# Performance work log

Measured on AMD Instinct MI355X. Metric: run time of the kernel, lower is better.

Reference implementation:

```python
import jax, jax.numpy as jnp
import numpy as np

B, T, L, D = 4, 64, 4096, 4096
MASK_VALUE = -1000000000.0


def setup_inputs() -> dict:
    key = jax.random.key(0)
    kq, km, ka = jax.random.split(key, 3)
    Q = jax.random.normal(kq, (1, T, D), dtype=jnp.float32)          # learned queries
    mask = jax.random.normal(km, (B, L, D), dtype=jnp.float32)       # acts as K and V
    attn_mask = jax.random.randint(ka, (B, T, L), 0, 2).astype(bool)  # True -> masked
    return {"mask": mask, "Q": Q, "attn_mask": attn_mask}


def reference(mask, Q, attn_mask):
    # scores: [B, T, L] = Q @ mask^T / sqrt(D)   (Q broadcast over batch)
    scale = 1.0 / np.sqrt(D).astype(np.float32)
    scores = jnp.einsum('td,bld->btl', Q[0], mask) * scale
    scores = jnp.where(attn_mask, MASK_VALUE, scores)
    attn = jax.nn.softmax(scores, axis=-1)
    # context: [B, T, D] = attn @ mask
    context = jnp.einsum('btl,bld->btd', attn, mask)
    return context
```

## Files before the change

### kernel.cpp

```cpp
#include <hip/hip_runtime.h>
#include <hip/hip_bf16.h>
#include <stdint.h>

#define B_ 4
#define T_ 64
#define L_ 4096
#define D_ 4096

using bf8   = __attribute__((ext_vector_type(8))) short;
using f32x4 = __attribute__((ext_vector_type(4))) float;

__device__ __forceinline__ unsigned short f2bf(float f) {
    union { float f; unsigned int u; } v;
    v.f = f;
    unsigned int r = v.u + 0x7fffu + ((v.u >> 16) & 1u);
    return (unsigned short)(r >> 16);
}

__device__ __forceinline__ int swz16(int row, int byteoff) {
    return byteoff ^ (((row ^ (row >> 3)) & 7) << 4);
}

__device__ __forceinline__ bf8 read_frag(const unsigned short* lds, int row, int kk, int lane) {
    int byte = kk * 64 + ((lane >> 4) << 4);
    int off  = row * 128 + swz16(row, byte);
    return *reinterpret_cast<const bf8*>(reinterpret_cast<const char*>(lds) + off);
}

__global__ __launch_bounds__(256) void k_qprep(const float* __restrict__ Q,
                                               unsigned short* __restrict__ Qbf) {
    int i = blockIdx.x * 256 + threadIdx.x;
    float4 f = reinterpret_cast<const float4*>(Q)[i];
    ushort4 u;
    u.x = f2bf(f.x); u.y = f2bf(f.y); u.z = f2bf(f.z); u.w = f2bf(f.w);
    reinterpret_cast<ushort4*>(Qbf)[i] = u;
}

__global__ __launch_bounds__(256, 1) void k_scores(
    const float* __restrict__ mask, const unsigned short* __restrict__ Qbf,
    float* __restrict__ scores) {
    __shared__ unsigned short lA[2][64 * 64];
    __shared__ unsigned short lB[2][64 * 64];
    const int tid  = threadIdx.x;
    const int lane = tid & 63;
    const int wave = tid >> 6;
    const int wm = wave >> 1, wn = wave & 1;
    const int b  = blockIdx.y;
    const int l0 = blockIdx.x * 64;
    const float* __restrict__ Mb = mask + (size_t)b * L_ * D_;

    f32x4 acc[2][2] = {};
    uint4  ra[2];
    float4 rb[4];

    const int NT    = D_ / 64;
    const int phase = blockIdx.x & (NT - 1);
    auto kof = [&](int kt) { int k = kt + phase; if (k >= NT) k -= NT; return k * 64; };

    auto loadTiles = [&](int k0) {
#pragma unroll
        for (int s = 0; s < 2; ++s) {
            int slot = tid + s * 256;
            int r = slot >> 3, c = slot & 7;
            ra[s] = *reinterpret_cast<const uint4*>(Qbf + (size_t)r * D_ + k0 + c * 8);
        }
#pragma unroll
        for (int s = 0; s < 4; ++s) {
            int slot = tid + s * 256;
            int r = slot >> 4, c = slot & 15;
            rb[s] = *reinterpret_cast<const float4*>(Mb + (size_t)(l0 + r) * D_ + k0 + c * 4);
        }
    };
    auto writeTiles = [&](int buf) {
#pragma unroll
        for (int s = 0; s < 2; ++s) {
            int slot = tid + s * 256;
            int r = slot >> 3, c = slot & 7;
            int off = r * 128 + swz16(r, c * 16);
            *reinterpret_cast<uint4*>(reinterpret_cast<char*>(lA[buf]) + off) = ra[s];
        }
#pragma unroll
        for (int s = 0; s < 4; ++s) {
            int slot = tid + s * 256;
            int r = slot >> 4, c = slot & 15;
            int off = r * 128 + swz16(r, c * 8);
            ushort4 u;
            u.x = f2bf(rb[s].x); u.y = f2bf(rb[s].y); u.z = f2bf(rb[s].z); u.w = f2bf(rb[s].w);
            *reinterpret_cast<ushort4*>(reinterpret_cast<char*>(lB[buf]) + off) = u;
        }
    };

    loadTiles(kof(0));
    writeTiles(0);
    __syncthreads();
    for (int kt = 0; kt < NT; ++kt) {
        int cur = kt & 1;
        if (kt + 1 < NT) loadTiles(kof(kt + 1));
#pragma unroll
        for (int kk = 0; kk < 2; ++kk) {
            bf8 a0 = read_frag(lA[cur], wm * 32 +      (lane & 15), kk, lane);
            bf8 a1 = read_frag(lA[cur], wm * 32 + 16 + (lane & 15), kk, lane);
            bf8 b0 = read_frag(lB[cur], wn * 32 +      (lane & 15), kk, lane);
            bf8 b1 = read_frag(lB[cur], wn * 32 + 16 + (lane & 15), kk, lane);
            acc[0][0] = __builtin_amdgcn_mfma_f32_16x16x32_bf16(a0, b0, acc[0][0], 0, 0, 0);
            acc[0][1] = __builtin_amdgcn_mfma_f32_16x16x32_bf16(a0, b1, acc[0][1], 0, 0, 0);
            acc[1][0] = __builtin_amdgcn_mfma_f32_16x16x32_bf16(a1, b0, acc[1][0], 0, 0, 0);
            acc[1][1] = __builtin_amdgcn_mfma_f32_16x16x32_bf16(a1, b1, acc[1][1], 0, 0, 0);
        }
        if (kt + 1 < NT) writeTiles(cur ^ 1);
        __syncthreads();
    }

    const int rgrp = (lane >> 4) * 4;
    const int cidx = lane & 15;
#pragma unroll
    for (int mi = 0; mi < 2; ++mi)
#pragma unroll
        for (int nj = 0; nj < 2; ++nj)
#pragma unroll
            for (int r = 0; r < 4; ++r) {
                int t = wm * 32 + mi * 16 + rgrp + r;
                int l = l0 + wn * 32 + nj * 16 + cidx;
                scores[((size_t)b * T_ + t) * L_ + l] = acc[mi][nj][r] * 0.015625f;
            }
}

__global__ __launch_bounds__(256, 4) void k_softmax(
    const float* __restrict__ scores, const int* __restrict__ am,
    unsigned short* __restrict__ attn) {
    const int row  = blockIdx.x;
    const int tid  = threadIdx.x;
    const int lane = tid & 63;
    const int wave = tid >> 6;
    const float* __restrict__ s = scores + (size_t)row * L_;
    const int*   __restrict__ m = am     + (size_t)row * L_;
    __shared__ float redmax[4], redsum[4];

    float v[16];
#pragma unroll
    for (int j = 0; j < 4; ++j) {
        float4 f = *(reinterpret_cast<const float4*>(s) + tid + j * 256);
        int4   q = *(reinterpret_cast<const int4*>(m)   + tid + j * 256);
        v[j * 4 + 0] = q.x ? -1.0e9f : f.x;
        v[j * 4 + 1] = q.y ? -1.0e9f : f.y;
        v[j * 4 + 2] = q.z ? -1.0e9f : f.z;
        v[j * 4 + 3] = q.w ? -1.0e9f : f.w;
    }
    float mx = -3.0e38f;
#pragma unroll
    for (int i = 0; i < 16; ++i) mx = fmaxf(mx, v[i]);
#pragma unroll
    for (int off = 32; off; off >>= 1) mx = fmaxf(mx, __shfl_xor(mx, off, 64));
    if (lane == 0) redmax[wave] = mx;
    __syncthreads();
    mx = fmaxf(fmaxf(redmax[0], redmax[1]), fmaxf(redmax[2], redmax[3]));

    float z = 0.f;
#pragma unroll
    for (int i = 0; i < 16; ++i) {
        v[i] = exp2f((v[i] - mx) * 1.4426950408889634f);
        z += v[i];
    }
#pragma unroll
    for (int off = 32; off; off >>= 1) z += __shfl_xor(z, off, 64);
    if (lane == 0) redsum[wave] = z;
    __syncthreads();
    z = (redsum[0] + redsum[1]) + (redsum[2] + redsum[3]);
    float inv = 1.0f / z;

    unsigned short* __restrict__ arow = attn + (size_t)row * L_;
#pragma unroll
    for (int j = 0; j < 4; ++j) {
        ushort4 u;
        u.x = f2bf(v[j * 4 + 0] * inv);
        u.y = f2bf(v[j * 4 + 1] * inv);
        u.z = f2bf(v[j * 4 + 2] * inv);
        u.w = f2bf(v[j * 4 + 3] * inv);
        *(reinterpret_cast<ushort4*>(arow) + tid + j * 256) = u;
    }
}

__global__ __launch_bounds__(256, 1) void k_context(
    const float* __restrict__ mask, const unsigned short* __restrict__ attn,
    float* __restrict__ out) {
    __shared__ unsigned short lA[2][64 * 64];
    __shared__ unsigned short lB[2][64 * 64];
    const int tid  = threadIdx.x;
    const int lane = tid & 63;
    const int wave = tid >> 6;
    const int wm = wave >> 1, wn = wave & 1;
    const int b  = blockIdx.y;
    const int d0 = blockIdx.x * 64;
    const float*          __restrict__ Mb = mask + (size_t)b * L_ * D_;
    const unsigned short* __restrict__ Ab = attn + (size_t)b * T_ * L_;

    f32x4 acc[2][2] = {};
    uint4  ra[2];
    float4 rb[4];

    const int NT    = L_ / 64;
    const int phase = blockIdx.x & (NT - 1);
    auto kof = [&](int kt) { int k = kt + phase; if (k >= NT) k -= NT; return k * 64; };

    auto loadTiles = [&](int k0) {
#pragma unroll
        for (int s = 0; s < 2; ++s) {
            int slot = tid + s * 256;
            int r = slot >> 3, c = slot & 7;
            ra[s] = *reinterpret_cast<const uint4*>(Ab + (size_t)r * L_ + k0 + c * 8);
        }
#pragma unroll
        for (int s = 0; s < 4; ++s) {
            int slot = tid + s * 256;
            int kl = slot >> 4, c = slot & 15;
            rb[s] = *reinterpret_cast<const float4*>(Mb + (size_t)(k0 + kl) * D_ + d0 + c * 4);
        }
    };
    auto writeTiles = [&](int buf) {
#pragma unroll
        for (int s = 0; s < 2; ++s) {
            int slot = tid + s * 256;
            int r = slot >> 3, c = slot & 7;
            int off = r * 128 + swz16(r, c * 16);
            *reinterpret_cast<uint4*>(reinterpret_cast<char*>(lA[buf]) + off) = ra[s];
        }
#pragma unroll
        for (int s = 0; s < 4; ++s) {
            int slot = tid + s * 256;
            int kl = slot >> 4, c = slot & 15;
            float fv[4] = { rb[s].x, rb[s].y, rb[s].z, rb[s].w };
#pragma unroll
            for (int i = 0; i < 4; ++i) {
                int d = c * 4 + i;
                int off = d * 128 + swz16(d, kl * 2);
                *reinterpret_cast<unsigned short*>(reinterpret_cast<char*>(lB[buf]) + off) = f2bf(fv[i]);
            }
        }
    };

    loadTiles(kof(0));
    writeTiles(0);
    __syncthreads();
    for (int kt = 0; kt < NT; ++kt) {
        int cur = kt & 1;
        if (kt + 1 < NT) loadTiles(kof(kt + 1));
#pragma unroll
        for (int kk = 0; kk < 2; ++kk) {
            bf8 a0 = read_frag(lA[cur], wm * 32 +      (lane & 15), kk, lane);
            bf8 a1 = read_frag(lA[cur], wm * 32 + 16 + (lane & 15), kk, lane);
            bf8 b0 = read_frag(lB[cur], wn * 32 +      (lane & 15), kk, lane);
            bf8 b1 = read_frag(lB[cur], wn * 32 + 16 + (lane & 15), kk, lane);
            acc[0][0] = __builtin_amdgcn_mfma_f32_16x16x32_bf16(a0, b0, acc[0][0], 0, 0, 0);
            acc[0][1] = __builtin_amdgcn_mfma_f32_16x16x32_bf16(a0, b1, acc[0][1], 0, 0, 0);
            acc[1][0] = __builtin_amdgcn_mfma_f32_16x16x32_bf16(a1, b0, acc[1][0], 0, 0, 0);
            acc[1][1] = __builtin_amdgcn_mfma_f32_16x16x32_bf16(a1, b1, acc[1][1], 0, 0, 0);
        }
        if (kt + 1 < NT) writeTiles(cur ^ 1);
        __syncthreads();
    }

    const int rgrp = (lane >> 4) * 4;
    const int cidx = lane & 15;
#pragma unroll
    for (int mi = 0; mi < 2; ++mi)
#pragma unroll
        for (int nj = 0; nj < 2; ++nj)
#pragma unroll
            for (int r = 0; r < 4; ++r) {
                int t = wm * 32 + mi * 16 + rgrp + r;
                int d = d0 + wn * 32 + nj * 16 + cidx;
                out[((size_t)b * T_ + t) * D_ + d] = acc[mi][nj][r];
            }
}

extern "C" void kernel_launch(void* const* d_in, const int* in_sizes, int n_in,
                              void* d_out, int out_size, void* d_ws, size_t ws_size,
                              hipStream_t stream) {
    const float* mask = (const float*)d_in[0];
    const float* Q    = (const float*)d_in[1];
    const int*   am   = (const int*)d_in[2];
    float* out = (float*)d_out;

    unsigned short* attn = (unsigned short*)d_ws;
    unsigned short* Qbf  = (unsigned short*)((char*)d_ws + (size_t)B_ * T_ * L_ * 2);

    k_qprep<<<dim3(T_ * D_ / 4 / 256), 256, 0, stream>>>(Q, Qbf);
    k_scores<<<dim3(L_ / 64, B_), 256, 0, stream>>>(mask, Qbf, out);
    k_softmax<<<dim3(B_ * T_), 256, 0, stream>>>(out, am, attn);
    k_context<<<dim3(D_ / 64, B_), 256, 0, stream>>>(mask, attn, out);
}
```

Before: 140.4 us.

## Fuse four phases into one cooperative kernel with grid syncs

Measured after the change: 332.1 us. +136.5%, slower.

```diff
diff --git a/kernel.cpp b/kernel.cpp
--- a/kernel.cpp
+++ b/kernel.cpp
@@ -1,6 +1,9 @@
 #include <hip/hip_runtime.h>
 #include <hip/hip_bf16.h>
+#include <hip/hip_cooperative_groups.h>
 #include <stdint.h>
+
+namespace cg = cooperative_groups;
 
 #define B_ 4
 #define T_ 64
@@ -27,35 +30,29 @@
     return *reinterpret_cast<const bf8*>(reinterpret_cast<const char*>(lds) + off);
 }
 
-__global__ __launch_bounds__(256) void k_qprep(const float* __restrict__ Q,
-                                               unsigned short* __restrict__ Qbf) {
-    int i = blockIdx.x * 256 + threadIdx.x;
+
+__device__ __forceinline__ void phase_qprep(const float* __restrict__ Q,
+                                            unsigned short* __restrict__ Qbf,
+                                            int bid, int tid) {
+    int i = bid * 256 + tid;
     float4 f = reinterpret_cast<const float4*>(Q)[i];
     ushort4 u;
     u.x = f2bf(f.x); u.y = f2bf(f.y); u.z = f2bf(f.z); u.w = f2bf(f.w);
     reinterpret_cast<ushort4*>(Qbf)[i] = u;
 }
 
-__global__ __launch_bounds__(256, 1) void k_scores(
+__device__ __forceinline__ void phase_scores(
     const float* __restrict__ mask, const unsigned short* __restrict__ Qbf,
-    float* __restrict__ scores) {
-    __shared__ unsigned short lA[2][64 * 64];
-    __shared__ unsigned short lB[2][64 * 64];
-    const int tid  = threadIdx.x;
+    float* __restrict__ scores, int b, int l0, int tid,
+    unsigned short (*lA)[64 * 64], unsigned short (*lB)[64 * 64]) {
     const int lane = tid & 63;
     const int wave = tid >> 6;
     const int wm = wave >> 1, wn = wave & 1;
-    const int b  = blockIdx.y;
-    const int l0 = blockIdx.x * 64;
     const float* __restrict__ Mb = mask + (size_t)b * L_ * D_;
 
     f32x4 acc[2][2] = {};
     uint4  ra[2];
     float4 rb[4];
-
-    const int NT    = D_ / 64;
-    const int phase = blockIdx.x & (NT - 1);
-    auto kof = [&](int kt) { int k = kt + phase; if (k >= NT) k -= NT; return k * 64; };
 
     auto loadTiles = [&](int k0) {
 #pragma unroll
@@ -90,12 +87,13 @@
         }
     };
 
-    loadTiles(kof(0));
+    loadTiles(0);
     writeTiles(0);
     __syncthreads();
+    const int NT = D_ / 64;
     for (int kt = 0; kt < NT; ++kt) {
         int cur = kt & 1;
-        if (kt + 1 < NT) loadTiles(kof(kt + 1));
+        if (kt + 1 < NT) loadTiles((kt + 1) * 64);
 #pragma unroll
         for (int kk = 0; kk < 2; ++kk) {
             bf8 a0 = read_frag(lA[cur], wm * 32 +      (lane & 15), kk, lane);
@@ -125,11 +123,9 @@
             }
 }
 
-__global__ __launch_bounds__(256, 4) void k_softmax(
+__device__ __forceinline__ void phase_softmax(
     const float* __restrict__ scores, const int* __restrict__ am,
-    unsigned short* __restrict__ attn) {
-    const int row  = blockIdx.x;
-    const int tid  = threadIdx.x;
+    unsigned short* __restrict__ attn, int row, int tid) {
     const int lane = tid & 63;
     const int wave = tid >> 6;
     const float* __restrict__ s = scores + (size_t)row * L_;
@@ -180,27 +176,19 @@
     }
 }
 
-__global__ __launch_bounds__(256, 1) void k_context(
+__device__ __forceinline__ void phase_context(
     const float* __restrict__ mask, const unsigned short* __restrict__ attn,
-    float* __restrict__ out) {
-    __shared__ unsigned short lA[2][64 * 64];
-    __shared__ unsigned short lB[2][64 * 64];
-    const int tid  = threadIdx.x;
+    float* __restrict__ out, int b, int d0, int tid,
+    unsigned short (*lA)[64 * 64], unsigned short (*lB)[64 * 64]) {
     const int lane = tid & 63;
     const int wave = tid >> 6;
     const int wm = wave >> 1, wn = wave & 1;
-    const int b  = blockIdx.y;
-    const int d0 = blockIdx.x * 64;
     const float*          __restrict__ Mb = mask + (size_t)b * L_ * D_;
     const unsigned short* __restrict__ Ab = attn + (size_t)b * T_ * L_;
 
     f32x4 acc[2][2] = {};
     uint4  ra[2];
     float4 rb[4];
-
-    const int NT    = L_ / 64;
-    const int phase = blockIdx.x & (NT - 1);
-    auto kof = [&](int kt) { int k = kt + phase; if (k >= NT) k -= NT; return k * 64; };
 
     auto loadTiles = [&](int k0) {
 #pragma unroll
@@ -238,12 +226,13 @@
         }
     };
 
-    loadTiles(kof(0));
+    loadTiles(0);
     writeTiles(0);
     __syncthreads();
+    const int NT = L_ / 64;
     for (int kt = 0; kt < NT; ++kt) {
         int cur = kt & 1;
-        if (kt + 1 < NT) loadTiles(kof(kt + 1));
+        if (kt + 1 < NT) loadTiles((kt + 1) * 64);
 #pragma unroll
         for (int kk = 0; kk < 2; ++kk) {
             bf8 a0 = read_frag(lA[cur], wm * 32 +      (lane & 15), kk, lane);
@@ -273,6 +262,50 @@
             }
 }
 
+__global__ __launch_bounds__(256, 1) void k_fused(
+    const float* __restrict__ mask, const float* __restrict__ Q,
+    const int* __restrict__ am, float* __restrict__ out,
+    unsigned short* __restrict__ attn, unsigned short* __restrict__ Qbf,
+    float* __restrict__ scores) {
+    __shared__ unsigned short lA[2][64 * 64];
+    __shared__ unsigned short lB[2][64 * 64];
+    cg::grid_group grid = cg::this_grid();
+    const int bid = blockIdx.x;
+    const int tid = threadIdx.x;
+
+    phase_qprep(Q, Qbf, bid, tid);
+    grid.sync();
+    phase_scores(mask, Qbf, scores, bid >> 6, (bid & 63) * 64, tid, lA, lB);
+    grid.sync();
+    phase_softmax(scores, am, attn, bid, tid);
+    grid.sync();
+    phase_context(mask, attn, out, bid >> 6, (bid & 63) * 64, tid, lA, lB);
+}
+
+__global__ __launch_bounds__(256) void k_qprep(const float* __restrict__ Q,
+                                               unsigned short* __restrict__ Qbf) {
+    phase_qprep(Q, Qbf, blockIdx.x, threadIdx.x);
+}
+__global__ __launch_bounds__(256, 1) void k_scores(const float* __restrict__ mask,
+                                                   const unsigned short* __restrict__ Qbf,
+                                                   float* __restrict__ scores) {
+    __shared__ unsigned short lA[2][64 * 64];
+    __shared__ unsigned short lB[2][64 * 64];
+    phase_scores(mask, Qbf, scores, blockIdx.y, blockIdx.x * 64, threadIdx.x, lA, lB);
+}
+__global__ __launch_bounds__(256, 4) void k_softmax(const float* __restrict__ scores,
+                                                    const int* __restrict__ am,
+                                                    unsigned short* __restrict__ attn) {
+    phase_softmax(scores, am, attn, blockIdx.x, threadIdx.x);
+}
+__global__ __launch_bounds__(256, 1) void k_context(const float* __restrict__ mask,
+                                                    const unsigned short* __restrict__ attn,
+                                                    float* __restrict__ out) {
+    __shared__ unsigned short lA[2][64 * 64];
+    __shared__ unsigned short lB[2][64 * 64];
+    phase_context(mask, attn, out, blockIdx.y, blockIdx.x * 64, threadIdx.x, lA, lB);
+}
+
 extern "C" void kernel_launch(void* const* d_in, const int* in_sizes, int n_in,
                               void* d_out, int out_size, void* d_ws, size_t ws_size,
                               hipStream_t stream) {
@@ -282,10 +315,17 @@
     float* out = (float*)d_out;
 
     unsigned short* attn = (unsigned short*)d_ws;
-    unsigned short* Qbf  = (unsigned short*)((char*)d_ws + (size_t)B_ * T_ * L_ * 2);
-
-    k_qprep<<<dim3(T_ * D_ / 4 / 256), 256, 0, stream>>>(Q, Qbf);
-    k_scores<<<dim3(L_ / 64, B_), 256, 0, stream>>>(mask, Qbf, out);
-    k_softmax<<<dim3(B_ * T_), 256, 0, stream>>>(out, am, attn);
-    k_context<<<dim3(D_ / 64, B_), 256, 0, stream>>>(mask, attn, out);
-}
+    unsigned short* Qbf  = (unsigned short*)((char*)d_ws + (2u << 20));
+    float*          scrs = (float*)((char*)d_ws + (2u << 20) + (512u << 10));
+
+    void* args[] = { (void*)&mask, (void*)&Q, (void*)&am, (void*)&out,
+                     (void*)&attn, (void*)&Qbf, (void*)&scrs };
+    hipError_t e = hipLaunchCooperativeKernel((const void*)k_fused, dim3(256), dim3(256),
+                                              args, 0, stream);
+    if (e != hipSuccess) {
+        k_qprep<<<dim3(T_ * D_ / 4 / 256), 256, 0, stream>>>(Q, Qbf);
+        k_scores<<<dim3(L_ / 64, B_), 256, 0, stream>>>(mask, Qbf, scrs);
+        k_softmax<<<dim3(B_ * T_), 256, 0, stream>>>(scrs, am, attn);
+        k_context<<<dim3(D_ / 64, B_), 256, 0, stream>>>(mask, attn, out);
+    }
+}
```
